# Optimization experiments

Measured on AMD Instinct MI355X. Metric: run time of the kernel, lower is better.

Reference implementation:

```python
import jax, jax.numpy as jnp
import numpy as np

B, L, D, C = 4, 512, 128, 128
EPS = 1e-7  # Keras backend epsilon


def setup_inputs() -> dict:
    key = jax.random.key(0)
    ks = jax.random.split(key, 4)
    inps = jax.random.normal(ks[0], (B, L, D), dtype=jnp.float32)
    # glorot_normal-ish scale for weights
    wei_t = jax.random.normal(ks[1], (D, C), dtype=jnp.float32) * (2.0 / (D + C)) ** 0.5
    wei_x = jax.random.normal(ks[2], (D, C), dtype=jnp.float32) * (2.0 / (D + C)) ** 0.5
    bxh = jnp.zeros((C,), dtype=jnp.float32)
    wei_a = jax.random.normal(ks[3], (C,), dtype=jnp.float32) * (2.0 / (C + 1)) ** 0.5
    bxa = jnp.zeros((), dtype=jnp.float32)
    return {"inps": inps, "wei_t": wei_t, "wei_x": wei_x, "bxh": bxh,
            "wei_a": wei_a, "bxa": bxa}


def reference(inps, wei_t, wei_x, bxh, wei_a, bxa):
    # Additive (Bahdanau-style) pairwise self-attention, no mask.
    qt = inps @ wei_t                      # [B, L, C] (query-side projection)
    kx = inps @ wei_x                      # [B, L, C] (key-side projection)
    # Pairwise hidden: [B, L, L, C]
    h = jnp.tanh(qt[:, :, None, :] + kx[:, None, :, :] + bxh)
    scores = jnp.einsum('bijc,c->bij', h, wei_a) + bxa  # [B, L, L]
    # activation_func=None -> linear (identity)
    e = jnp.exp(scores - jnp.max(scores, axis=-1, keepdims=True))
    a = e / (jnp.sum(e, axis=-1, keepdims=True) + EPS)   # [B, L, L]
    out = jnp.einsum('bij,bjd->bid', a, inps)            # [B, L, D]
    return out
```

## Files before the change

kernel.cpp:

```cpp
#include <hip/hip_runtime.h>

#define NB 4
#define SL 512
#define DD 128
#define CC 128

__device__ __forceinline__ float fexp2(float x) { return __builtin_amdgcn_exp2f(x); }
__device__ __forceinline__ float frcp(float x)  { return __builtin_amdgcn_rcpf(x); }

__global__ __launch_bounds__(512) void proj_kernel(
    const float* __restrict__ inps, const float* __restrict__ wei_t,
    const float* __restrict__ wei_x, const float* __restrict__ bxh,
    float* __restrict__ E, float* __restrict__ F)
{
    __shared__ float part[2 * 128 * 5];
    const float K2 = 2.8853900817779268f;
    const int row0 = blockIdx.x * 4;
    const int b    = row0 >> 9;
    const int i0   = row0 & 511;
    const int tid  = threadIdx.x;
    const int c    = tid & 127;
    const int sel  = (tid >> 7) & 1;
    const int kh   = tid >> 8;

    const float* W = (sel ? wei_x : wei_t) + kh * 64 * CC;
    const float* r = inps + (size_t)row0 * DD + kh * 64;

    float a0 = 0.f, a1 = 0.f, a2 = 0.f, a3 = 0.f;
    #pragma unroll 16
    for (int k = 0; k < 64; ++k) {
        float w = W[k * CC + c];
        a0 = fmaf(r[k         ], w, a0);
        a1 = fmaf(r[DD     + k], w, a1);
        a2 = fmaf(r[2 * DD + k], w, a2);
        a3 = fmaf(r[3 * DD + k], w, a3);
    }

    if (kh == 1) {
        float* m = &part[(sel * 128 + c) * 5];
        m[0] = a0; m[1] = a1; m[2] = a2; m[3] = a3;
    }
    __syncthreads();
    if (kh == 0) {
        const float* m = &part[(sel * 128 + c) * 5];
        a0 += m[0]; a1 += m[1]; a2 += m[2]; a3 += m[3];
        if (sel == 0) {
            float bb = bxh[c];
            E[(size_t)(row0 + 0) * CC + c] = fexp2(K2 * (a0 + bb));
            E[(size_t)(row0 + 1) * CC + c] = fexp2(K2 * (a1 + bb));
            E[(size_t)(row0 + 2) * CC + c] = fexp2(K2 * (a2 + bb));
            E[(size_t)(row0 + 3) * CC + c] = fexp2(K2 * (a3 + bb));
        } else {
            float4 v = {fexp2(K2 * a0), fexp2(K2 * a1), fexp2(K2 * a2), fexp2(K2 * a3)};
            *reinterpret_cast<float4*>(&F[((size_t)b * CC + c) * SL + i0]) = v;
        }
    }
}

__global__ __launch_bounds__(1024, 8) void attn_kernel(
    const float* __restrict__ inps, const float* __restrict__ wei_a,
    const float* __restrict__ E, const float* __restrict__ F,
    float* __restrict__ out)
{
    __shared__ float4 upk[CC];
    __shared__ float pool[4 * 16 * DD];
    __shared__ float scT[SL * 4];
    __shared__ float redw[4 * 4];

    const int blk = blockIdx.x;
    const int b   = blk >> 7;
    const int i0  = (blk & 127) * 4;
    const int bi0 = b * SL + i0;
    const int tid = threadIdx.x;
    const int jt  = tid & 255;
    const int cq  = tid >> 8;
    const int j0  = jt * 2;

    if (tid < CC) {
        float4 u;
        u.x = E[(size_t)(bi0 + 0) * CC + tid];
        u.y = E[(size_t)(bi0 + 1) * CC + tid];
        u.z = E[(size_t)(bi0 + 2) * CC + tid];
        u.w = E[(size_t)(bi0 + 3) * CC + tid];
        upk[tid] = u;
    }
    __syncthreads();

    const int c0 = cq * 32;
    const float* fb = F + ((size_t)b * CC + c0) * SL + j0;
    const float4* up = upk + c0;
    const float* wa = wei_a + c0;
    float sx[4] = {0.f, 0.f, 0.f, 0.f};
    float sy[4] = {0.f, 0.f, 0.f, 0.f};
    #pragma unroll 4
    for (int cp = 0; cp < 16; ++cp) {
        float2 f0 = *reinterpret_cast<const float2*>(&fb[(size_t)(2 * cp) * SL]);
        float2 f1 = *reinterpret_cast<const float2*>(&fb[(size_t)(2 * cp + 1) * SL]);
        float4 u0 = up[2 * cp];
        float4 u1 = up[2 * cp + 1];
        float wa0 = wa[2 * cp], wa1 = wa[2 * cp + 1];
        const float* u0p = reinterpret_cast<const float*>(&u0);
        const float* u1p = reinterpret_cast<const float*>(&u1);
        #pragma unroll
        for (int i = 0; i < 4; ++i) {
            float ax = fmaf(u0p[i], f0.x, 1.0f);
            float bx = fmaf(u1p[i], f1.x, 1.0f);
            float numx = fmaf(wa0, bx, wa1 * ax);
            sx[i] = fmaf(numx, frcp(ax * bx), sx[i]);
            float ay = fmaf(u0p[i], f0.y, 1.0f);
            float by = fmaf(u1p[i], f1.y, 1.0f);
            float numy = fmaf(wa0, by, wa1 * ay);
            sy[i] = fmaf(numy, frcp(ay * by), sy[i]);
        }
    }

    if (cq > 0) {
        float* m = &pool[(cq - 1) * 2304 + jt * 9];
        #pragma unroll
        for (int i = 0; i < 4; ++i) { m[i] = sx[i]; m[4 + i] = sy[i]; }
    }
    __syncthreads();

    if (cq == 0) {
        #pragma unroll
        for (int seg = 0; seg < 3; ++seg) {
            const float* m = &pool[seg * 2304 + jt * 9];
            #pragma unroll
            for (int i = 0; i < 4; ++i) { sx[i] += m[i]; sy[i] += m[4 + i]; }
        }
        const float KE = -2.8853900817779268f;
        float ex[4], ey[4];
        const int lane = tid & 63, wv = tid >> 6;
        #pragma unroll
        for (int i = 0; i < 4; ++i) {
            ex[i] = fexp2(sx[i] * KE);
            ey[i] = fexp2(sy[i] * KE);
            float t = ex[i] + ey[i];
            #pragma unroll
            for (int off = 32; off > 0; off >>= 1)
                t += __shfl_xor(t, off, 64);
            if (lane == 0) redw[i * 4 + wv] = t;
        }
        __syncthreads();
        float4 av0, av1;
        {
            float S0 = redw[0] + redw[1] + redw[2] + redw[3];
            float S1 = redw[4] + redw[5] + redw[6] + redw[7];
            float S2 = redw[8] + redw[9] + redw[10] + redw[11];
            float S3 = redw[12] + redw[13] + redw[14] + redw[15];
            float r0 = frcp(S0 + 1e-7f), r1 = frcp(S1 + 1e-7f);
            float r2 = frcp(S2 + 1e-7f), r3 = frcp(S3 + 1e-7f);
            av0 = make_float4(ex[0] * r0, ex[1] * r1, ex[2] * r2, ex[3] * r3);
            av1 = make_float4(ey[0] * r0, ey[1] * r1, ey[2] * r2, ey[3] * r3);
        }
        *reinterpret_cast<float4*>(&scT[j0 * 4])     = av0;
        *reinterpret_cast<float4*>(&scT[j0 * 4 + 4]) = av1;
    } else {
        __syncthreads();
    }
    __syncthreads();

    if (tid < 512) {
        const int dq = (tid & 31) * 4;
        const int jq = tid >> 5;
        const float* ibase = inps + (size_t)b * SL * DD;
        float4 acc0 = {0,0,0,0}, acc1 = {0,0,0,0}, acc2 = {0,0,0,0}, acc3 = {0,0,0,0};
        const int jb = jq * 32;
        #pragma unroll 4
        for (int jj = 0; jj < 32; ++jj) {
            int jx = jb + jj;
            float4 v  = *reinterpret_cast<const float4*>(ibase + (size_t)jx * DD + dq);
            float4 a4 = *reinterpret_cast<const float4*>(&scT[jx * 4]);
            acc0.x = fmaf(a4.x, v.x, acc0.x); acc0.y = fmaf(a4.x, v.y, acc0.y);
            acc0.z = fmaf(a4.x, v.z, acc0.z); acc0.w = fmaf(a4.x, v.w, acc0.w);
            acc1.x = fmaf(a4.y, v.x, acc1.x); acc1.y = fmaf(a4.y, v.y, acc1.y);
            acc1.z = fmaf(a4.y, v.z, acc1.z); acc1.w = fmaf(a4.y, v.w, acc1.w);
            acc2.x = fmaf(a4.z, v.x, acc2.x); acc2.y = fmaf(a4.z, v.y, acc2.y);
            acc2.z = fmaf(a4.z, v.z, acc2.z); acc2.w = fmaf(a4.z, v.w, acc2.w);
            acc3.x = fmaf(a4.w, v.x, acc3.x); acc3.y = fmaf(a4.w, v.y, acc3.y);
            acc3.z = fmaf(a4.w, v.z, acc3.z); acc3.w = fmaf(a4.w, v.w, acc3.w);
        }
        *reinterpret_cast<float4*>(&pool[(0 * 16 + jq) * DD + dq]) = acc0;
        *reinterpret_cast<float4*>(&pool[(1 * 16 + jq) * DD + dq]) = acc1;
        *reinterpret_cast<float4*>(&pool[(2 * 16 + jq) * DD + dq]) = acc2;
        *reinterpret_cast<float4*>(&pool[(3 * 16 + jq) * DD + dq]) = acc3;
    }
    __syncthreads();
    if (tid < 512) {
        int i = tid >> 7, d = tid & 127;
        float sum = 0.f;
        #pragma unroll
        for (int q = 0; q < 16; ++q) sum += pool[(i * 16 + q) * DD + d];
        out[(size_t)(bi0 + i) * DD + d] = sum;
    }
}

extern "C" void kernel_launch(void* const* d_in, const int* in_sizes, int n_in,
                              void* d_out, int out_size, void* d_ws, size_t ws_size,
                              hipStream_t stream) {
    const float* inps  = (const float*)d_in[0];
    const float* wei_t = (const float*)d_in[1];
    const float* wei_x = (const float*)d_in[2];
    const float* bxh   = (const float*)d_in[3];
    const float* wei_a = (const float*)d_in[4];
    float* out = (float*)d_out;

    float* E = (float*)d_ws;
    float* F = E + (size_t)NB * SL * CC;

    proj_kernel<<<NB * SL / 4, 512, 0, stream>>>(inps, wei_t, wei_x, bxh, E, F);
    attn_kernel<<<NB * SL / 4, 1024, 0, stream>>>(inps, wei_a, E, F, out);
}
```

Measured before the change: 94.17 us.

## Fuse projection and attention into one cooperative kernel with grid syncs

Replaces the two-kernel pipeline with a single cooperative kernel. Each block computes its own query-side exp projection straight into shared memory and writes its slice of the key-side projection into the output buffer, which doubles as scratch. A grid-wide sync separates the projection stage from the score stage, and a second one makes sure all key-side reads finish before the output is overwritten. The softmax and the weighted-sum stages are also respread across all 1024 threads instead of one quarter or one half of them. It falls back to the original two kernels if the cooperative launch fails, trading a kernel boundary for two grid barriers and a residency requirement of two blocks per CU.

Measured after the change: 233.1 us. +147.6%, slower.

```diff
diff --git a/kernel.cpp b/kernel.cpp
--- a/kernel.cpp
+++ b/kernel.cpp
@@ -1,4 +1,7 @@
 #include <hip/hip_runtime.h>
+#include <hip/hip_cooperative_groups.h>
+
+namespace cg = cooperative_groups;
 
 #define NB 4
 #define SL 512
@@ -7,6 +10,146 @@
 
 __device__ __forceinline__ float fexp2(float x) { return __builtin_amdgcn_exp2f(x); }
 __device__ __forceinline__ float frcp(float x)  { return __builtin_amdgcn_rcpf(x); }
+
+__global__ __launch_bounds__(1024, 8) void fused_kernel(
+    const float* __restrict__ inps, const float* __restrict__ wei_t,
+    const float* __restrict__ wei_x, const float* __restrict__ bxh,
+    const float* __restrict__ wei_a, float* __restrict__ outF)
+{
+    __shared__ float4 upk[CC];
+    __shared__ float pool[4 * 32 * DD];
+    __shared__ float scT[SL * 4];
+    __shared__ float redw[4 * 4];
+
+    const float K2 = 2.8853900817779268f;
+    const int blk = blockIdx.x;
+    const int b   = blk >> 7;
+    const int i0  = (blk & 127) * 4;
+    const int bi0 = b * SL + i0;
+    const int tid = threadIdx.x;
+
+    {
+        const int mat = tid >> 9;
+        const int r   = (tid >> 7) & 3;
+        const int c   = tid & 127;
+        const float* W  = mat ? wei_x : wei_t;
+        const float* rp = inps + (size_t)(bi0 + r) * DD;
+        float acc = 0.f;
+        #pragma unroll 16
+        for (int k = 0; k < DD; ++k)
+            acc = fmaf(rp[k], W[k * CC + c], acc);
+        if (mat == 0) {
+            ((float*)&upk[c])[r] = fexp2(K2 * (acc + bxh[c]));
+        } else {
+            pool[c * 5 + r] = fexp2(K2 * acc);
+        }
+    }
+    __syncthreads();
+    if (tid < CC) {
+        float4 f = {pool[tid * 5 + 0], pool[tid * 5 + 1],
+                    pool[tid * 5 + 2], pool[tid * 5 + 3]};
+        *reinterpret_cast<float4*>(&outF[((size_t)b * CC + tid) * SL + i0]) = f;
+    }
+    cg::this_grid().sync();
+
+    const int jt = tid & 255;
+    const int cq = tid >> 8;
+    const int j0 = jt * 2;
+    const int c0 = cq * 32;
+    const float* fb = outF + ((size_t)b * CC + c0) * SL + j0;
+    const float4* up = upk + c0;
+    const float* wa = wei_a + c0;
+    float sx[4] = {0.f, 0.f, 0.f, 0.f};
+    float sy[4] = {0.f, 0.f, 0.f, 0.f};
+    #pragma unroll 4
+    for (int cp = 0; cp < 16; ++cp) {
+        float2 f0 = *reinterpret_cast<const float2*>(&fb[(size_t)(2 * cp) * SL]);
+        float2 f1 = *reinterpret_cast<const float2*>(&fb[(size_t)(2 * cp + 1) * SL]);
+        float4 u0 = up[2 * cp];
+        float4 u1 = up[2 * cp + 1];
+        float wa0 = wa[2 * cp], wa1 = wa[2 * cp + 1];
+        const float* u0p = reinterpret_cast<const float*>(&u0);
+        const float* u1p = reinterpret_cast<const float*>(&u1);
+        #pragma unroll
+        for (int i = 0; i < 4; ++i) {
+            float ax = fmaf(u0p[i], f0.x, 1.0f);
+            float bx = fmaf(u1p[i], f1.x, 1.0f);
+            float numx = fmaf(wa0, bx, wa1 * ax);
+            sx[i] = fmaf(numx, frcp(ax * bx), sx[i]);
+            float ay = fmaf(u0p[i], f0.y, 1.0f);
+            float by = fmaf(u1p[i], f1.y, 1.0f);
+            float numy = fmaf(wa0, by, wa1 * ay);
+            sy[i] = fmaf(numy, frcp(ay * by), sy[i]);
+        }
+    }
+    {
+        float* m = &pool[cq * 2304 + jt * 9];
+        #pragma unroll
+        for (int i = 0; i < 4; ++i) { m[i] = sx[i]; m[4 + i] = sy[i]; }
+    }
+    __syncthreads();
+
+    {
+        const int jp = tid & 255;
+        const int i  = tid >> 8;
+        float sxx = 0.f, syy = 0.f;
+        #pragma unroll
+        for (int seg = 0; seg < 4; ++seg) {
+            const float* m = &pool[seg * 2304 + jp * 9];
+            sxx += m[i]; syy += m[4 + i];
+        }
+        const float KE = -2.8853900817779268f;
+        float ex = fexp2(sxx * KE);
+        float ey = fexp2(syy * KE);
+        float t = ex + ey;
+        #pragma unroll
+        for (int off = 32; off > 0; off >>= 1)
+            t += __shfl_xor(t, off, 64);
+        if ((tid & 63) == 0) redw[i * 4 + ((tid >> 6) & 3)] = t;
+        __syncthreads();
+        float S = redw[i * 4 + 0] + redw[i * 4 + 1]
+                + redw[i * 4 + 2] + redw[i * 4 + 3];
+        float rS = frcp(S + 1e-7f);
+        scT[(jp * 2    ) * 4 + i] = ex * rS;
+        scT[(jp * 2 + 1) * 4 + i] = ey * rS;
+    }
+    __syncthreads();
+
+    {
+        const int dq = (tid & 31) * 4;
+        const int jq = tid >> 5;
+        const float* ibase = inps + (size_t)b * SL * DD;
+        float4 acc0 = {0,0,0,0}, acc1 = {0,0,0,0}, acc2 = {0,0,0,0}, acc3 = {0,0,0,0};
+        const int jb = jq * 16;
+        #pragma unroll 4
+        for (int jj = 0; jj < 16; ++jj) {
+            int jx = jb + jj;
+            float4 v  = *reinterpret_cast<const float4*>(ibase + (size_t)jx * DD + dq);
+            float4 a4 = *reinterpret_cast<const float4*>(&scT[jx * 4]);
+            acc0.x = fmaf(a4.x, v.x, acc0.x); acc0.y = fmaf(a4.x, v.y, acc0.y);
+            acc0.z = fmaf(a4.x, v.z, acc0.z); acc0.w = fmaf(a4.x, v.w, acc0.w);
+            acc1.x = fmaf(a4.y, v.x, acc1.x); acc1.y = fmaf(a4.y, v.y, acc1.y);
+            acc1.z = fmaf(a4.y, v.z, acc1.z); acc1.w = fmaf(a4.y, v.w, acc1.w);
+            acc2.x = fmaf(a4.z, v.x, acc2.x); acc2.y = fmaf(a4.z, v.y, acc2.y);
+            acc2.z = fmaf(a4.z, v.z, acc2.z); acc2.w = fmaf(a4.z, v.w, acc2.w);
+            acc3.x = fmaf(a4.w, v.x, acc3.x); acc3.y = fmaf(a4.w, v.y, acc3.y);
+            acc3.z = fmaf(a4.w, v.z, acc3.z); acc3.w = fmaf(a4.w, v.w, acc3.w);
+        }
+        *reinterpret_cast<float4*>(&pool[(0 * 32 + jq) * DD + dq]) = acc0;
+        *reinterpret_cast<float4*>(&pool[(1 * 32 + jq) * DD + dq]) = acc1;
+        *reinterpret_cast<float4*>(&pool[(2 * 32 + jq) * DD + dq]) = acc2;
+        *reinterpret_cast<float4*>(&pool[(3 * 32 + jq) * DD + dq]) = acc3;
+    }
+    cg::this_grid().sync();
+
+    if (tid < 512) {
+        int i = tid >> 7, d = tid & 127;
+        float sum = 0.f;
+        #pragma unroll
+        for (int q = 0; q < 32; ++q) sum += pool[(i * 32 + q) * DD + d];
+        outF[(size_t)(bi0 + i) * DD + d] = sum;
+    }
+}
 
 __global__ __launch_bounds__(512) void proj_kernel(
     const float* __restrict__ inps, const float* __restrict__ wei_t,
@@ -35,7 +178,6 @@
         a2 = fmaf(r[2 * DD + k], w, a2);
         a3 = fmaf(r[3 * DD + k], w, a3);
     }
-
     if (kh == 1) {
         float* m = &part[(sel * 128 + c) * 5];
         m[0] = a0; m[1] = a1; m[2] = a2; m[3] = a3;
@@ -113,7 +255,6 @@
             sy[i] = fmaf(numy, frcp(ay * by), sy[i]);
         }
     }
-
     if (cq > 0) {
         float* m = &pool[(cq - 1) * 2304 + jt * 9];
         #pragma unroll
@@ -205,9 +346,14 @@
     const float* wei_a = (const float*)d_in[4];
     float* out = (float*)d_out;
 
-    float* E = (float*)d_ws;
-    float* F = E + (size_t)NB * SL * CC;
-
-    proj_kernel<<<NB * SL / 4, 512, 0, stream>>>(inps, wei_t, wei_x, bxh, E, F);
-    attn_kernel<<<NB * SL / 4, 1024, 0, stream>>>(inps, wei_a, E, F, out);
+    void* args[] = {(void*)&inps, (void*)&wei_t, (void*)&wei_x,
+                    (void*)&bxh, (void*)&wei_a, (void*)&out};
+    hipError_t err = hipLaunchCooperativeKernel(
+        (const void*)fused_kernel, dim3(NB * SL / 4), dim3(1024), args, 0, stream);
+    if (err != hipSuccess) {
+        float* E = (float*)d_ws;
+        float* F = E + (size_t)NB * SL * CC;
+        proj_kernel<<<NB * SL / 4, 512, 0, stream>>>(inps, wei_t, wei_x, bxh, E, F);
+        attn_kernel<<<NB * SL / 4, 1024, 0, stream>>>(inps, wei_a, E, F, out);
+    }
 }
```

## Spread softmax and output accumulation across all 1024 threads in attention kernel

Applied to the files above, without the earlier changes.

The softmax stage now uses every thread: each of the four warps-groups handles one query row and reduces the four channel partials itself, instead of leaving three quarters of the block idle while one quarter does all rows. The weighted-sum stage also uses all 1024 threads with half the j-range each, which doubles the shared pool used for the final reduction. The occupancy hint in launch bounds drops from 8 to 4, and the larger shared footprint (about 64KB for pool) may cut how many blocks fit per CU.

After: 96.80 us. 2.8% more time.

```diff
diff --git a/kernel.cpp b/kernel.cpp
--- a/kernel.cpp
+++ b/kernel.cpp
@@ -57,13 +57,13 @@
     }
 }
 
-__global__ __launch_bounds__(1024, 8) void attn_kernel(
+__global__ __launch_bounds__(1024, 4) void attn_kernel(
     const float* __restrict__ inps, const float* __restrict__ wei_a,
     const float* __restrict__ E, const float* __restrict__ F,
     float* __restrict__ out)
 {
     __shared__ float4 upk[CC];
-    __shared__ float pool[4 * 16 * DD];
+    __shared__ float pool[4 * 32 * DD];
     __shared__ float scT[SL * 4];
     __shared__ float redw[4 * 4];
 
@@ -113,61 +113,47 @@
             sy[i] = fmaf(numy, frcp(ay * by), sy[i]);
         }
     }
-
-    if (cq > 0) {
-        float* m = &pool[(cq - 1) * 2304 + jt * 9];
+    {
+        float* m = &pool[cq * 2304 + jt * 9];
         #pragma unroll
         for (int i = 0; i < 4; ++i) { m[i] = sx[i]; m[4 + i] = sy[i]; }
     }
     __syncthreads();
 
-    if (cq == 0) {
-        #pragma unroll
-        for (int seg = 0; seg < 3; ++seg) {
-            const float* m = &pool[seg * 2304 + jt * 9];
-            #pragma unroll
-            for (int i = 0; i < 4; ++i) { sx[i] += m[i]; sy[i] += m[4 + i]; }
+    {
+        const int jp = tid & 255;
+        const int i  = tid >> 8;
+        float sxx = 0.f, syy = 0.f;
+        #pragma unroll
+        for (int seg = 0; seg < 4; ++seg) {
+            const float* m = &pool[seg * 2304 + jp * 9];
+            sxx += m[i]; syy += m[4 + i];
         }
         const float KE = -2.8853900817779268f;
-        float ex[4], ey[4];
-        const int lane = tid & 63, wv = tid >> 6;
-        #pragma unroll
-        for (int i = 0; i < 4; ++i) {
-            ex[i] = fexp2(sx[i] * KE);
-            ey[i] = fexp2(sy[i] * KE);
-            float t = ex[i] + ey[i];
-            #pragma unroll
-            for (int off = 32; off > 0; off >>= 1)
-                t += __shfl_xor(t, off, 64);
-            if (lane == 0) redw[i * 4 + wv] = t;
-        }
+        float ex = fexp2(sxx * KE);
+        float ey = fexp2(syy * KE);
+        float t = ex + ey;
+        #pragma unroll
+        for (int off = 32; off > 0; off >>= 1)
+            t += __shfl_xor(t, off, 64);
+        if ((tid & 63) == 0) redw[i * 4 + ((tid >> 6) & 3)] = t;
         __syncthreads();
-        float4 av0, av1;
-        {
-            float S0 = redw[0] + redw[1] + redw[2] + redw[3];
-            float S1 = redw[4] + redw[5] + redw[6] + redw[7];
-            float S2 = redw[8] + redw[9] + redw[10] + redw[11];
-            float S3 = redw[12] + redw[13] + redw[14] + redw[15];
-            float r0 = frcp(S0 + 1e-7f), r1 = frcp(S1 + 1e-7f);
-            float r2 = frcp(S2 + 1e-7f), r3 = frcp(S3 + 1e-7f);
-            av0 = make_float4(ex[0] * r0, ex[1] * r1, ex[2] * r2, ex[3] * r3);
-            av1 = make_float4(ey[0] * r0, ey[1] * r1, ey[2] * r2, ey[3] * r3);
-        }
-        *reinterpret_cast<float4*>(&scT[j0 * 4])     = av0;
-        *reinterpret_cast<float4*>(&scT[j0 * 4 + 4]) = av1;
-    } else {
-        __syncthreads();
-    }
-    __syncthreads();
-
-    if (tid < 512) {
+        float S = redw[i * 4 + 0] + redw[i * 4 + 1]
+                + redw[i * 4 + 2] + redw[i * 4 + 3];
+        float rS = frcp(S + 1e-7f);
+        scT[(jp * 2    ) * 4 + i] = ex * rS;
+        scT[(jp * 2 + 1) * 4 + i] = ey * rS;
+    }
+    __syncthreads();
+
+    {
         const int dq = (tid & 31) * 4;
         const int jq = tid >> 5;
         const float* ibase = inps + (size_t)b * SL * DD;
         float4 acc0 = {0,0,0,0}, acc1 = {0,0,0,0}, acc2 = {0,0,0,0}, acc3 = {0,0,0,0};
-        const int jb = jq * 32;
+        const int jb = jq * 16;
         #pragma unroll 4
-        for (int jj = 0; jj < 32; ++jj) {
+        for (int jj = 0; jj < 16; ++jj) {
             int jx = jb + jj;
             float4 v  = *reinterpret_cast<const float4*>(ibase + (size_t)jx * DD + dq);
             float4 a4 = *reinterpret_cast<const float4*>(&scT[jx * 4]);
@@ -180,17 +166,18 @@
             acc3.x = fmaf(a4.w, v.x, acc3.x); acc3.y = fmaf(a4.w, v.y, acc3.y);
             acc3.z = fmaf(a4.w, v.z, acc3.z); acc3.w = fmaf(a4.w, v.w, acc3.w);
         }
-        *reinterpret_cast<float4*>(&pool[(0 * 16 + jq) * DD + dq]) = acc0;
-        *reinterpret_cast<float4*>(&pool[(1 * 16 + jq) * DD + dq]) = acc1;
-        *reinterpret_cast<float4*>(&pool[(2 * 16 + jq) * DD + dq]) = acc2;
-        *reinterpret_cast<float4*>(&pool[(3 * 16 + jq) * DD + dq]) = acc3;
-    }
-    __syncthreads();
+        *reinterpret_cast<float4*>(&pool[(0 * 32 + jq) * DD + dq]) = acc0;
+        *reinterpret_cast<float4*>(&pool[(1 * 32 + jq) * DD + dq]) = acc1;
+        *reinterpret_cast<float4*>(&pool[(2 * 32 + jq) * DD + dq]) = acc2;
+        *reinterpret_cast<float4*>(&pool[(3 * 32 + jq) * DD + dq]) = acc3;
+    }
+    __syncthreads();
+
     if (tid < 512) {
         int i = tid >> 7, d = tid & 127;
         float sum = 0.f;
         #pragma unroll
-        for (int q = 0; q < 16; ++q) sum += pool[(i * 16 + q) * DD + d];
+        for (int q = 0; q < 32; ++q) sum += pool[(i * 32 + q) * DD + d];
         out[(size_t)(bi0 + i) * DD + d] = sum;
     }
 }
```
